# Performance work log

Measured on AMD Instinct MI355X. Metric: run time of the kernel, lower is better.

Reference implementation:

```python
import jax, jax.numpy as jnp
import numpy as np

B, S, D, H, HD, FF, L = 16384, 5, 6, 2, 3, 2048, 4
EPS = 1e-5


def setup_inputs() -> dict:
    key = jax.random.key(0)
    ks = jax.random.split(key, 20)
    s = lambda fan: 1.0 / np.sqrt(fan)
    inp = {
        'x': jax.random.normal(ks[0], (B, S, D), dtype=jnp.float32),
        # per-layer stacked MHA params (in_proj split into q/k/v) and out_proj
        'Wq': jax.random.uniform(ks[1], (L, D, D), jnp.float32, -s(D), s(D)),
        'bq': jax.random.uniform(ks[2], (L, D), jnp.float32, -s(D), s(D)),
        'Wk': jax.random.uniform(ks[3], (L, D, D), jnp.float32, -s(D), s(D)),
        'bk': jax.random.uniform(ks[4], (L, D), jnp.float32, -s(D), s(D)),
        'Wv': jax.random.uniform(ks[5], (L, D, D), jnp.float32, -s(D), s(D)),
        'bv': jax.random.uniform(ks[6], (L, D), jnp.float32, -s(D), s(D)),
        'Wo': jax.random.uniform(ks[7], (L, D, D), jnp.float32, -s(D), s(D)),
        'bo': jax.random.uniform(ks[8], (L, D), jnp.float32, -s(D), s(D)),
        # FFN: linear1 D->FF, linear2 FF->D (torch Linear stores [out,in])
        'W1': jax.random.uniform(ks[9], (L, FF, D), jnp.float32, -s(D), s(D)),
        'b1': jax.random.uniform(ks[10], (L, FF), jnp.float32, -s(D), s(D)),
        'W2': jax.random.uniform(ks[11], (L, D, FF), jnp.float32, -s(FF), s(FF)),
        'b2': jax.random.uniform(ks[12], (L, D), jnp.float32, -s(FF), s(FF)),
        # layernorms
        'g1': jnp.ones((L, D), jnp.float32),
        'be1': jnp.zeros((L, D), jnp.float32),
        'g2': jnp.ones((L, D), jnp.float32),
        'be2': jnp.zeros((L, D), jnp.float32),
        # classification head Linear(30, 2)
        'Wfc': jax.random.uniform(ks[13], (2, S * D), jnp.float32, -s(S * D), s(S * D)),
        'bfc': jax.random.uniform(ks[14], (2,), jnp.float32, -s(S * D), s(S * D)),
    }
    return inp


def _layernorm(x, g, b):
    m = jnp.mean(x, axis=-1, keepdims=True)
    v = jnp.mean(jnp.square(x - m), axis=-1, keepdims=True)
    return (x - m) * jax.lax.rsqrt(v + EPS) * g + b


def _encoder_stack(x, Wq, bq, Wk, bk, Wv, bv, Wo, bo, W1, b1, W2, b2, g1, be1, g2, be2):
    scale = 1.0 / np.sqrt(HD)
    for i in range(L):  # small fixed loop over layers
        # multi-head self-attention (post-norm, eval mode: dropout = identity)
        q = (x @ Wq[i].T + bq[i]).reshape(B, S, H, HD)
        k = (x @ Wk[i].T + bk[i]).reshape(B, S, H, HD)
        v = (x @ Wv[i].T + bv[i]).reshape(B, S, H, HD)
        scores = jnp.einsum('bqhd,bkhd->bhqk', q, k) * scale
        attn = jax.nn.softmax(scores, axis=-1)
        ctx = jnp.einsum('bhqk,bkhd->bqhd', attn, v).reshape(B, S, D)
        x = _layernorm(x + ctx @ Wo[i].T + bo[i], g1[i], be1[i])
        # FFN: relu(x W1^T + b1) W2^T + b2
        h = jax.nn.relu(x @ W1[i].T + b1[i])  # [B,S,FF]
        x = _layernorm(x + h @ W2[i].T + b2[i], g2[i], be2[i])
    return x


def reference(x, Wq, bq, Wk, bk, Wv, bv, Wo, bo, W1, b1, W2, b2, g1, be1, g2, be2, Wfc, bfc):
    t = _encoder_stack(x, Wq, bq, Wk, bk, Wv, bv, Wo, bo, W1, b1, W2, b2, g1, be1, g2, be2)
    flat = t.reshape(-1, S * D)
    logits = flat @ Wfc.T + bfc
    return jax.nn.softmax(logits, axis=1)
```

## Files before the change

### kernel.cpp

```cpp
#include <hip/hip_runtime.h>
#include <math.h>

#define NL 4
#define NBATCH 16384
#define NS 5
#define ND 6
#define NH 2
#define NHD 3
#define NFF 2048
#define EPSV 1e-5f

#define ITEMS 16
#define TPB 256
#define NPAIR 64
#define ROW (NS * ND)
#define NVAL (ITEMS * ROW)

typedef __fp16 v8h __attribute__((ext_vector_type(8)));
typedef __fp16 v2h __attribute__((ext_vector_type(2)));
typedef float f32x4 __attribute__((ext_vector_type(4)));

union HU8 { uint4 u; v8h h; __fp16 f[8]; };

__device__ inline unsigned pk_u32(float a, float b) {
    union { v2h h; unsigned u; } x;
    x.h = __builtin_amdgcn_cvt_pkrtz(a, b);
    return x.u;
}

__device__ __align__(16) uint4 W1A[NL * NPAIR * 64];
__device__ __align__(16) uint4 W1B[NL * NPAIR * 64];
__device__ __align__(16) uint4 W2P[NL * NPAIR * 64];

__global__ void pack_kernel(const float* __restrict__ W1,
                            const float* __restrict__ b1,
                            const float* __restrict__ W2) {
    const int TOT = NL * NPAIR * 64;
    int idx = blockIdx.x * 256 + threadIdx.x;
    if (idx >= 3 * TOT) return;
    int arr = idx / TOT, t = idx - arr * TOT;
    int lane = t & 63, p = (t >> 6) & 63, l = t >> 12;
    int r = lane & 15, g = lane >> 4;
    HU8 o; o.u = make_uint4(0u, 0u, 0u, 0u);
    if (arr < 2) {
        if (g == 0) {
            int j = (2 * p + arr) * 16 + r;
#pragma unroll
            for (int e = 0; e < ND; ++e)
                o.f[e] = (__fp16)W1[(size_t)(l * NFF + j) * ND + e];
            o.f[6] = (__fp16)b1[l * NFF + j];
            o.f[7] = (__fp16)0.f;
        }
        if (arr == 0) W1A[t] = o.u; else W1B[t] = o.u;
    } else {
        if (r < ND) {
#pragma unroll
            for (int e = 0; e < 8; ++e) {
                int j = p * 32 + ((e < 4) ? (4 * g + e) : (16 + 4 * g + e - 4));
                o.f[e] = (__fp16)W2[(size_t)(l * ND + r) * NFF + j];
            }
        }
        W2P[t] = o.u;
    }
}

__global__ __launch_bounds__(TPB, 4) void encoder_kernel(
    const float* __restrict__ xin,
    const float* __restrict__ Wq, const float* __restrict__ bq,
    const float* __restrict__ Wk, const float* __restrict__ bk,
    const float* __restrict__ Wv, const float* __restrict__ bv,
    const float* __restrict__ Wo, const float* __restrict__ bo,
    const float* __restrict__ b2,
    const float* __restrict__ g1, const float* __restrict__ be1,
    const float* __restrict__ g2, const float* __restrict__ be2,
    const float* __restrict__ Wfc, const float* __restrict__ bfc,
    float* __restrict__ out) {
    __shared__ float xs[NVAL];
    __shared__ float ybuf[4 * 5 * 32 * 4];
    __shared__ float kvs[ITEMS * NS * 2 * ND];

    const int tid = threadIdx.x;
    const int base = blockIdx.x * ITEMS;

    if (tid < NVAL / 4)
        ((float4*)xs)[tid] = ((const float4*)(xin + (size_t)base * ROW))[tid];
    __syncthreads();

    const bool act = tid < ITEMS * NS;
    const int ai = tid / NS;
    const int at = tid - ai * NS;

    const int lane = tid & 63;
    const int jq = tid >> 6;
    const int c16 = lane & 15, g = lane >> 4;

    v8h z8; z8 = (v8h)(__fp16)0.f;
    const f32x4 cz = {0.f, 0.f, 0.f, 0.f};

    for (int l = 0; l < NL; ++l) {
        const uint4* pw1a = W1A + (size_t)(l * NPAIR + jq * 16) * 64 + lane;
        const uint4* pw1b = W1B + (size_t)(l * NPAIR + jq * 16) * 64 + lane;
        const uint4* pw2  = W2P + (size_t)(l * NPAIR + jq * 16) * 64 + lane;
        uint4 wpf[2][6];
#pragma unroll
        for (int pp = 0; pp < 2; ++pp) {
            wpf[0][pp * 3 + 0] = pw1a[pp * 64];
            wpf[0][pp * 3 + 1] = pw1b[pp * 64];
            wpf[0][pp * 3 + 2] = pw2[pp * 64];
        }

        float xr[ND], qv[ND];
        if (act) {
#pragma unroll
            for (int d = 0; d < ND; ++d) xr[d] = xs[(ai * NS + at) * ND + d];
#pragma unroll
            for (int d = 0; d < ND; ++d) {
                float aq = bq[l * ND + d], ak = bk[l * ND + d], av = bv[l * ND + d];
#pragma unroll
                for (int e = 0; e < ND; ++e) {
                    aq += Wq[(l * ND + d) * ND + e] * xr[e];
                    ak += Wk[(l * ND + d) * ND + e] * xr[e];
                    av += Wv[(l * ND + d) * ND + e] * xr[e];
                }
                qv[d] = aq;
                kvs[(ai * NS + at) * 2 * ND + d] = ak;
                kvs[(ai * NS + at) * 2 * ND + ND + d] = av;
            }
        }
        __syncthreads();
        if (act) {
            const float scale = 0.57735026919f;
            float ctx[ND];
#pragma unroll
            for (int h = 0; h < NH; ++h) {
                float sc[NS];
                float mx = -1e30f;
#pragma unroll
                for (int u = 0; u < NS; ++u) {
                    float s = 0.f;
#pragma unroll
                    for (int d = 0; d < NHD; ++d)
                        s += qv[h * NHD + d] * kvs[(ai * NS + u) * 2 * ND + h * NHD + d];
                    s *= scale;
                    sc[u] = s;
                    mx = fmaxf(mx, s);
                }
                float sum = 0.f;
#pragma unroll
                for (int u = 0; u < NS; ++u) {
                    sc[u] = __expf(sc[u] - mx);
                    sum += sc[u];
                }
                float inv = 1.f / sum;
#pragma unroll
                for (int d = 0; d < NHD; ++d) {
                    float cx = 0.f;
#pragma unroll
                    for (int u = 0; u < NS; ++u)
                        cx += sc[u] * kvs[(ai * NS + u) * 2 * ND + ND + h * NHD + d];
                    ctx[h * NHD + d] = cx * inv;
                }
            }
            float yr[ND];
#pragma unroll
            for (int d = 0; d < ND; ++d) {
                float a = bo[l * ND + d];
#pragma unroll
                for (int e = 0; e < ND; ++e) a += Wo[(l * ND + d) * ND + e] * ctx[e];
                yr[d] = a + xr[d];
            }
            float m = 0.f;
#pragma unroll
            for (int d = 0; d < ND; ++d) m += yr[d];
            m *= (1.f / ND);
            float va = 0.f;
#pragma unroll
            for (int d = 0; d < ND; ++d) { float dv = yr[d] - m; va += dv * dv; }
            va *= (1.f / ND);
            float r = rsqrtf(va + EPSV);
#pragma unroll
            for (int d = 0; d < ND; ++d)
                xs[(ai * NS + at) * ND + d] =
                    (yr[d] - m) * r * g1[l * ND + d] + be1[l * ND + d];
        }
        __syncthreads();
        v8h xb[5];
#pragma unroll
        for (int mt = 0; mt < 5; ++mt) {
            HU8 ux; ux.u = make_uint4(0u, 0u, 0u, 0u);
            if (g == 0) {
                int row = mt * 16 + c16;
                const float* xp = &xs[row * ND];
                ux.u.x = pk_u32(xp[0], xp[1]);
                ux.u.y = pk_u32(xp[2], xp[3]);
                ux.u.z = pk_u32(xp[4], xp[5]);
                ux.u.w = 0x00003c00u;
            }
            xb[mt] = ux.h;
        }
        f32x4 y0 = cz, y1 = cz, y2 = cz, y3 = cz, y4 = cz;
        __builtin_amdgcn_s_setprio(1);
#pragma unroll
        for (int gq = 0; gq < 8; ++gq) {
            const int cur = gq & 1, nxt = cur ^ 1;
            if (gq < 7) {
#pragma unroll
                for (int pp = 0; pp < 2; ++pp) {
                    int pofs = (gq * 2 + 2 + pp) * 64;
                    wpf[nxt][pp * 3 + 0] = pw1a[pofs];
                    wpf[nxt][pp * 3 + 1] = pw1b[pofs];
                    wpf[nxt][pp * 3 + 2] = pw2[pofs];
                }
            }
#pragma unroll
            for (int pp = 0; pp < 2; ++pp) {
                HU8 a1; a1.u = wpf[cur][pp * 3 + 0];
                HU8 b1f; b1f.u = wpf[cur][pp * 3 + 1];
                HU8 w2f; w2f.u = wpf[cur][pp * 3 + 2];
#define FFN_STEP(YREG, XB)                                                      \
                {                                                               \
                    f32x4 h0 = __builtin_amdgcn_mfma_f32_16x16x32_f16(          \
                        a1.h, (XB), cz, 0, 0, 0);                               \
                    f32x4 h1 = __builtin_amdgcn_mfma_f32_16x16x32_f16(          \
                        b1f.h, (XB), cz, 0, 0, 0);                              \
                    HU8 hb;                                                     \
                    hb.u.x = pk_u32(h0.x, h0.y);                                \
                    hb.u.y = pk_u32(h0.z, h0.w);                                \
                    hb.u.z = pk_u32(h1.x, h1.y);                                \
                    hb.u.w = pk_u32(h1.z, h1.w);                                \
                    hb.h = __builtin_elementwise_max(hb.h, z8);                 \
                    YREG = __builtin_amdgcn_mfma_f32_16x16x32_f16(              \
                        w2f.h, hb.h, YREG, 0, 0, 0);                            \
                }
                FFN_STEP(y0, xb[0])
                FFN_STEP(y1, xb[1])
                FFN_STEP(y2, xb[2])
                FFN_STEP(y3, xb[3])
                FFN_STEP(y4, xb[4])
#undef FFN_STEP
            }
        }
        __builtin_amdgcn_s_setprio(0);
        if (lane < 32) {
            f32x4* yb4 = (f32x4*)ybuf;
            int sb = (jq * 5) * 32 + lane;
            yb4[sb + 0 * 32] = y0;
            yb4[sb + 1 * 32] = y1;
            yb4[sb + 2 * 32] = y2;
            yb4[sb + 3 * 32] = y3;
            yb4[sb + 4 * 32] = y4;
        }
        __syncthreads();
        if (act) {
            int R = ai * NS + at;
            int mtR = R >> 4, cR = R & 15;
            float yr[ND];
#pragma unroll
            for (int d = 0; d < ND; ++d) {
                int gR = d >> 2, iR = d & 3;
                float s = 0.f;
#pragma unroll
                for (int q = 0; q < 4; ++q)
                    s += ybuf[((q * 5 + mtR) * 32 + gR * 16 + cR) * 4 + iR];
                yr[d] = xs[R * ND + d] + s + b2[l * ND + d];
            }
            float m = 0.f;
#pragma unroll
            for (int d = 0; d < ND; ++d) m += yr[d];
            m *= (1.f / ND);
            float va = 0.f;
#pragma unroll
            for (int d = 0; d < ND; ++d) { float dv = yr[d] - m; va += dv * dv; }
            va *= (1.f / ND);
            float r = rsqrtf(va + EPSV);
#pragma unroll
            for (int d = 0; d < ND; ++d)
                xs[R * ND + d] = (yr[d] - m) * r * g2[l * ND + d] + be2[l * ND + d];
        }
        __syncthreads();
    }
    if (tid < ITEMS) {
        float l0 = bfc[0], l1 = bfc[1];
#pragma unroll
        for (int v = 0; v < ROW; ++v) {
            float xv = xs[tid * ROW + v];
            l0 += Wfc[v] * xv;
            l1 += Wfc[ROW + v] * xv;
        }
        float mx = fmaxf(l0, l1);
        float e0 = __expf(l0 - mx), e1 = __expf(l1 - mx);
        float inv = 1.f / (e0 + e1);
        out[(size_t)(base + tid) * 2 + 0] = e0 * inv;
        out[(size_t)(base + tid) * 2 + 1] = e1 * inv;
    }
}

extern "C" void kernel_launch(void* const* d_in, const int* in_sizes, int n_in,
                              void* d_out, int out_size, void* d_ws, size_t ws_size,
                              hipStream_t stream) {
    (void)in_sizes; (void)n_in; (void)d_ws; (void)ws_size; (void)out_size;
    const float* x = (const float*)d_in[0];
    const float* Wq = (const float*)d_in[1];
    const float* bq = (const float*)d_in[2];
    const float* Wk = (const float*)d_in[3];
    const float* bk = (const float*)d_in[4];
    const float* Wv = (const float*)d_in[5];
    const float* bv = (const float*)d_in[6];
    const float* Wo = (const float*)d_in[7];
    const float* bo = (const float*)d_in[8];
    const float* W1 = (const float*)d_in[9];
    const float* b1 = (const float*)d_in[10];
    const float* W2 = (const float*)d_in[11];
    const float* b2 = (const float*)d_in[12];
    const float* g1 = (const float*)d_in[13];
    const float* be1 = (const float*)d_in[14];
    const float* g2 = (const float*)d_in[15];
    const float* be2 = (const float*)d_in[16];
    const float* Wfc = (const float*)d_in[17];
    const float* bfc = (const float*)d_in[18];
    float* out = (float*)d_out;

    const int npack = 3 * NL * NPAIR * 64;
    hipLaunchKernelGGL(pack_kernel, dim3((npack + 255) / 256), dim3(256), 0, stream,
                       W1, b1, W2);
    hipLaunchKernelGGL(encoder_kernel, dim3(NBATCH / ITEMS), dim3(TPB), 0, stream,
                       x, Wq, bq, Wk, bk, Wv, bv, Wo, bo, b2, g1, be1, g2, be2,
                       Wfc, bfc, out);
}
```

Measured before the change: 64.40 us.

## Compact packed FFN weights and load only nonzero lanes with deeper prefetch

Measured after the change: 71.27 us. +10.7%, slower.

```diff
diff --git a/kernel.cpp b/kernel.cpp
--- a/kernel.cpp
+++ b/kernel.cpp
@@ -16,6 +16,9 @@
 #define ROW (NS * ND)
 #define NVAL (ITEMS * ROW)
 
+#define W1K_N (NL * NPAIR * 2 * 16)
+#define W2K_N (NL * NPAIR * 4 * 6)
+
 typedef __fp16 v8h __attribute__((ext_vector_type(8)));
 typedef __fp16 v2h __attribute__((ext_vector_type(2)));
 typedef float f32x4 __attribute__((ext_vector_type(4)));
@@ -27,44 +30,44 @@
     x.h = __builtin_amdgcn_cvt_pkrtz(a, b);
     return x.u;
 }
-
-__device__ __align__(16) uint4 W1A[NL * NPAIR * 64];
-__device__ __align__(16) uint4 W1B[NL * NPAIR * 64];
-__device__ __align__(16) uint4 W2P[NL * NPAIR * 64];
+__device__ inline unsigned packh(float a, float b) {
+    union { __fp16 h[2]; unsigned u; } x;
+    x.h[0] = (__fp16)a; x.h[1] = (__fp16)b; return x.u;
+}
+
+__device__ __align__(16) uint4 W1K[W1K_N];
+__device__ __align__(16) uint4 W2K[W2K_N + 64];
 
 __global__ void pack_kernel(const float* __restrict__ W1,
                             const float* __restrict__ b1,
                             const float* __restrict__ W2) {
-    const int TOT = NL * NPAIR * 64;
     int idx = blockIdx.x * 256 + threadIdx.x;
-    if (idx >= 3 * TOT) return;
-    int arr = idx / TOT, t = idx - arr * TOT;
-    int lane = t & 63, p = (t >> 6) & 63, l = t >> 12;
-    int r = lane & 15, g = lane >> 4;
-    HU8 o; o.u = make_uint4(0u, 0u, 0u, 0u);
-    if (arr < 2) {
-        if (g == 0) {
-            int j = (2 * p + arr) * 16 + r;
-#pragma unroll
-            for (int e = 0; e < ND; ++e)
-                o.f[e] = (__fp16)W1[(size_t)(l * NFF + j) * ND + e];
-            o.f[6] = (__fp16)b1[l * NFF + j];
-            o.f[7] = (__fp16)0.f;
-        }
-        if (arr == 0) W1A[t] = o.u; else W1B[t] = o.u;
-    } else {
-        if (r < ND) {
-#pragma unroll
-            for (int e = 0; e < 8; ++e) {
-                int j = p * 32 + ((e < 4) ? (4 * g + e) : (16 + 4 * g + e - 4));
-                o.f[e] = (__fp16)W2[(size_t)(l * ND + r) * NFF + j];
-            }
-        }
-        W2P[t] = o.u;
+    if (idx < W1K_N) {
+        int r = idx & 15, t = (idx >> 4) & 1, p = (idx >> 5) & 63, l = idx >> 11;
+        int j = (2 * p + t) * 16 + r;
+        uint4 o;
+        o.x = packh(W1[(size_t)(l * NFF + j) * ND + 0], W1[(size_t)(l * NFF + j) * ND + 1]);
+        o.y = packh(W1[(size_t)(l * NFF + j) * ND + 2], W1[(size_t)(l * NFF + j) * ND + 3]);
+        o.z = packh(W1[(size_t)(l * NFF + j) * ND + 4], W1[(size_t)(l * NFF + j) * ND + 5]);
+        o.w = packh(b1[l * NFF + j], 0.f);
+        W1K[idx] = o;
+    } else if (idx < W1K_N + W2K_N) {
+        int t = idx - W1K_N;
+        int r = t % 6; int t6 = t / 6;
+        int g = t6 & 3, p = (t6 >> 2) & 63, l = t6 >> 8;
+        HU8 o;
+#pragma unroll
+        for (int e = 0; e < 8; ++e) {
+            int j = p * 32 + ((e < 4) ? (4 * g + e) : (16 + 4 * g + e - 4));
+            o.f[e] = (__fp16)W2[(size_t)(l * ND + r) * NFF + j];
+        }
+        W2K[t] = o.u;
     }
 }
 
-__global__ __launch_bounds__(TPB, 4) void encoder_kernel(
+__global__ __launch_bounds__(TPB)
+__attribute__((amdgpu_waves_per_eu(4, 4)))
+void encoder_kernel(
     const float* __restrict__ xin,
     const float* __restrict__ Wq, const float* __restrict__ bq,
     const float* __restrict__ Wk, const float* __restrict__ bk,
@@ -96,18 +99,24 @@
 
     v8h z8; z8 = (v8h)(__fp16)0.f;
     const f32x4 cz = {0.f, 0.f, 0.f, 0.f};
+    const uint4 u4z = make_uint4(0u, 0u, 0u, 0u);
 
     for (int l = 0; l < NL; ++l) {
-        const uint4* pw1a = W1A + (size_t)(l * NPAIR + jq * 16) * 64 + lane;
-        const uint4* pw1b = W1B + (size_t)(l * NPAIR + jq * 16) * 64 + lane;
-        const uint4* pw2  = W2P + (size_t)(l * NPAIR + jq * 16) * 64 + lane;
-        uint4 wpf[2][6];
-#pragma unroll
-        for (int pp = 0; pp < 2; ++pp) {
-            wpf[0][pp * 3 + 0] = pw1a[pp * 64];
-            wpf[0][pp * 3 + 1] = pw1b[pp * 64];
-            wpf[0][pp * 3 + 2] = pw2[pp * 64];
-        }
+        const uint4* p1 = W1K + (size_t)(l * NPAIR + jq * 16) * 32 + c16;
+        const uint4* p2 = W2K + ((size_t)(l * NPAIR + jq * 16) * 4 + g) * 6 + c16;
+        uint4 wa[2][2], wb[2][2], ww[2][2];
+#pragma unroll
+        for (int bb = 0; bb < 2; ++bb)
+#pragma unroll
+            for (int pp = 0; pp < 2; ++pp) {
+                const int pr = bb * 2 + pp;
+                wa[bb][pp] = u4z; wb[bb][pp] = u4z; ww[bb][pp] = u4z;
+                if (g == 0) {
+                    wa[bb][pp] = p1[pr * 32];
+                    wb[bb][pp] = p1[pr * 32 + 16];
+                }
+                if (c16 < 6) ww[bb][pp] = p2[pr * 24];
+            }
 
         float xr[ND], qv[ND];
         if (act) {
@@ -187,7 +196,7 @@
         v8h xb[5];
 #pragma unroll
         for (int mt = 0; mt < 5; ++mt) {
-            HU8 ux; ux.u = make_uint4(0u, 0u, 0u, 0u);
+            HU8 ux; ux.u = u4z;
             if (g == 0) {
                 int row = mt * 16 + c16;
                 const float* xp = &xs[row * ND];
@@ -202,21 +211,12 @@
         __builtin_amdgcn_s_setprio(1);
 #pragma unroll
         for (int gq = 0; gq < 8; ++gq) {
-            const int cur = gq & 1, nxt = cur ^ 1;
-            if (gq < 7) {
-#pragma unroll
-                for (int pp = 0; pp < 2; ++pp) {
-                    int pofs = (gq * 2 + 2 + pp) * 64;
-                    wpf[nxt][pp * 3 + 0] = pw1a[pofs];
-                    wpf[nxt][pp * 3 + 1] = pw1b[pofs];
-                    wpf[nxt][pp * 3 + 2] = pw2[pofs];
-                }
-            }
+            const int cur = gq & 1;
 #pragma unroll
             for (int pp = 0; pp < 2; ++pp) {
-                HU8 a1; a1.u = wpf[cur][pp * 3 + 0];
-                HU8 b1f; b1f.u = wpf[cur][pp * 3 + 1];
-                HU8 w2f; w2f.u = wpf[cur][pp * 3 + 2];
+                HU8 a1; a1.u = wa[cur][pp];
+                HU8 b1f; b1f.u = wb[cur][pp];
+                HU8 w2f; w2f.u = ww[cur][pp];
 #define FFN_STEP(YREG, XB)                                                      \
                 {                                                               \
                     f32x4 h0 = __builtin_amdgcn_mfma_f32_16x16x32_f16(          \
@@ -238,6 +238,19 @@
                 FFN_STEP(y3, xb[3])
                 FFN_STEP(y4, xb[4])
 #undef FFN_STEP
+            }
+            if (gq < 6) {
+#pragma unroll
+                for (int pp = 0; pp < 2; ++pp) {
+                    const int pr = (gq + 2) * 2 + pp;
+                    uint4 na = u4z, nb = u4z, nw = u4z;
+                    if (g == 0) {
+                        na = p1[pr * 32];
+                        nb = p1[pr * 32 + 16];
+                    }
+                    if (c16 < 6) nw = p2[pr * 24];
+                    wa[cur][pp] = na; wb[cur][pp] = nb; ww[cur][pp] = nw;
+                }
             }
         }
         __builtin_amdgcn_s_setprio(0);
@@ -320,7 +333,7 @@
     const float* bfc = (const float*)d_in[18];
     float* out = (float*)d_out;
 
-    const int npack = 3 * NL * NPAIR * 64;
+    const int npack = W1K_N + W2K_N;
     hipLaunchKernelGGL(pack_kernel, dim3((npack + 255) / 256), dim3(256), 0, stream,
                        W1, b1, W2);
     hipLaunchKernelGGL(encoder_kernel, dim3(NBATCH / ITEMS), dim3(TPB), 0, stream,
```
